# Performance work log

Hardware: AMD Instinct MI355X
Metric: run time of the kernel (lower is better)

The kernel has to match this reference:

```python
import jax, jax.numpy as jnp
import numpy as np
import math

B, N, DQK, DV, M = 8, 8192, 128, 128, 256


def _make_omega(m: int, d: int, seed: int = 0) -> jnp.ndarray:
    """Block-orthogonal random feature matrix, shape [d, m] (matches torch _omega)."""
    rng = np.random.default_rng(seed)
    blocks = []
    nblocks = m // d
    for _ in range(nblocks):
        q, _ = np.linalg.qr(rng.standard_normal((d, d)))
        blocks.append(q.T)
    missing = m - nblocks * d
    if missing > 0:
        q, _ = np.linalg.qr(rng.standard_normal((d, d)))
        blocks.append(q.T[:missing])
    norm = np.linalg.norm(rng.standard_normal((m, d)), axis=1, keepdims=True)
    omega = (norm * np.vstack(blocks)).T  # [d, m]
    return jnp.asarray(omega, dtype=jnp.float32)


def setup_inputs() -> dict:
    key = jax.random.key(0)
    kq, kk, kv = jax.random.split(key, 3)
    Q = jax.random.normal(kq, (B, N, DQK), jnp.float32)
    K = jax.random.normal(kk, (B, N, DQK), jnp.float32)
    V = jax.random.normal(kv, (B, N, DV), jnp.float32)
    atom_mask = jnp.ones((B, N), jnp.float32)
    omega = _make_omega(M, DQK)
    return {"Q": Q, "K": K, "V": V, "atom_mask": atom_mask, "omega": omega}


def _phi(X, mask, omega, is_query: bool, eps: float = 1e-4):
    """Project into random-feature space with Performer stabilization."""
    d = X.shape[-1]
    m = omega.shape[-1]
    U = (X / d ** 0.25) @ omega                       # [B, N, m]
    h = jnp.sum(X * X, axis=-1, keepdims=True) / (2.0 * d ** 0.5)
    if is_query:
        mx = jnp.max(U, axis=-1, keepdims=True)       # per-token max
    else:
        mx = jnp.max(U, axis=(-2, -1), keepdims=True)  # per-batch max
    return (jnp.exp(U - h - mx) + eps) / math.sqrt(m) * mask[..., None]


def reference(Q, K, V, atom_mask, omega):
    eps = 1e-8
    Qp = _phi(Q, atom_mask, omega, True)   # [B, N, M]
    Kp = _phi(K, atom_mask, omega, False)  # [B, N, M]
    # norm_n = Qp_n . sum_j Kp_j
    norm = jnp.einsum('bnm,bm->bn', Qp, jnp.sum(Kp, axis=1))[..., None] + eps
    KV = jnp.einsum('bnm,bnv->bmv', Kp, V)             # [B, M, DV]
    return jnp.einsum('bnm,bmv->bnv', Qp, KV) / norm   # [B, N, DV]
```

## Files before the change

### kernel.cpp

```cpp
#include <hip/hip_runtime.h>
#include <math.h>

#define BB 8
#define NN 8192
#define DD 128
#define MM 256
#define DVV 128
#define PP 32
#define CHUNK 32

#define XSCALE 0.29730177875068026f
#define INV_SQRT_M 0.0625f

typedef _Float16 f16x8 __attribute__((ext_vector_type(8)));
typedef float f32x16 __attribute__((ext_vector_type(16)));

#define FR(s, l) ((s) * 520 + (l) * 8)

__device__ __forceinline__ unsigned f2ord(float f) {
    unsigned u = __float_as_uint(f);
    return (u & 0x80000000u) ? ~u : (u | 0x80000000u);
}
__device__ __forceinline__ float ord2f(unsigned u) {
    return (u & 0x80000000u) ? __uint_as_float(u & 0x7fffffffu) : __uint_as_float(~u);
}
__device__ __forceinline__ f32x16 mfma16(f16x8 a, f16x8 b, f32x16 c) {
    return __builtin_amdgcn_mfma_f32_32x32x16_f16(a, b, c, 0, 0, 0);
}
__device__ __forceinline__ int rowf(int r, int q) { return (r & 3) + 8 * (r >> 2) + 4 * q; }

__device__ __forceinline__ void stage_A(const float* __restrict__ src,
                                        _Float16* R1, float* hs, float* msk,
                                        const float* __restrict__ mrow, bool do_h) {
    const int tid = threadIdx.x;
    const int t = tid >> 3, ks = tid & 7;
    const float4* s4 = (const float4*)(src + t * DD + ks * 16);
    float x[16];
    #pragma unroll
    for (int u = 0; u < 4; ++u) {
        float4 v = s4[u];
        x[u*4+0] = v.x * XSCALE; x[u*4+1] = v.y * XSCALE;
        x[u*4+2] = v.z * XSCALE; x[u*4+3] = v.w * XSCALE;
    }
    if (do_h) {
        float p = 0.f;
        #pragma unroll
        for (int u = 0; u < 16; ++u) p += x[u] * x[u];
        p += __shfl_xor(p, 1, 64); p += __shfl_xor(p, 2, 64); p += __shfl_xor(p, 4, 64);
        if (ks == 0) { hs[t] = 0.5f * p; msk[t] = mrow[t]; }
    }
    #pragma unroll
    for (int q = 0; q < 2; ++q) {
        f16x8 h8, l8;
        #pragma unroll
        for (int j = 0; j < 8; ++j) {
            float xv = x[q*8 + j];
            _Float16 h = (_Float16)xv;
            h8[j] = h; l8[j] = (_Float16)(xv - (float)h);
        }
        *(f16x8*)&R1[FR(0*8 + ks, q*32 + t)] = h8;
        *(f16x8*)&R1[FR(1*8 + ks, q*32 + t)] = l8;
    }
}

__device__ __forceinline__ void stage_BV(const float* __restrict__ src, _Float16* R1) {
    const int tid = threadIdx.x;
    const int t = tid >> 3, c0 = (tid & 7) * 16;
    const int ts = t >> 4, qq = (t >> 3) & 1, j = t & 7;
    const float4* s4 = (const float4*)(src + t * DVV + c0);
    #pragma unroll
    for (int u = 0; u < 4; ++u) {
        float4 v = s4[u];
        float vv[4] = {v.x, v.y, v.z, v.w};
        #pragma unroll
        for (int e = 0; e < 4; ++e) {
            int c = c0 + u*4 + e;
            int vt = c >> 5, iv = c & 31;
            _Float16 h = (_Float16)vv[e];
            R1[FR((0*4 + vt)*2 + ts, qq*32 + iv) + j] = h;
            R1[FR((1*4 + vt)*2 + ts, qq*32 + iv) + j] = (_Float16)(vv[e] - (float)h);
        }
    }
}

__global__ __launch_bounds__(256) void pack_kernel(const float* __restrict__ omega,
                                                   _Float16* __restrict__ omh,
                                                   _Float16* __restrict__ oml,
                                                   unsigned* __restrict__ kmaxord) {
    int g = blockIdx.x * 256 + threadIdx.x;
    if (g < BB) kmaxord[g] = f2ord(-INFINITY);
    int lane = g & 63, ks = (g >> 6) & 7, nt = g >> 9;
    int q = lane >> 5, i = lane & 31;
    f16x8 h8, l8;
    #pragma unroll
    for (int j = 0; j < 8; ++j) {
        float w = omega[(size_t)(ks*16 + q*8 + j) * MM + nt*32 + i];
        _Float16 h = (_Float16)w;
        h8[j] = h; l8[j] = (_Float16)(w - (float)h);
    }
    ((f16x8*)omh)[g] = h8;
    ((f16x8*)oml)[g] = l8;
}

__global__ __launch_bounds__(256, 2) void kmax_kernel(const float* __restrict__ K,
                                                      const _Float16* __restrict__ omh,
                                                      unsigned* __restrict__ kmaxord) {
    __shared__ __align__(16) _Float16 R1[16 * 520];
    __shared__ float wred[4];
    const int b = blockIdx.y;
    const int tid = threadIdx.x, w = tid >> 6, lane = tid & 63;

    f16x8 om[2][8];
    #pragma unroll
    for (int n = 0; n < 2; ++n)
        #pragma unroll
        for (int k = 0; k < 8; ++k)
            om[n][k] = ((const f16x8*)omh)[((2*w + n)*8 + k)*64 + lane];

    float mx = -INFINITY;
    for (int c = 0; c < 8; ++c) {
        int t0 = (blockIdx.x * 8 + c) * CHUNK;
        __syncthreads();
        stage_A(K + ((size_t)b*NN + t0) * DD, R1, nullptr, nullptr, nullptr, false);
        __syncthreads();
        f32x16 a0, a1;
        #pragma unroll
        for (int r = 0; r < 16; ++r) { a0[r] = 0.f; a1[r] = 0.f; }
        #pragma unroll
        for (int ks = 0; ks < 8; ++ks) {
            f16x8 ah = *(const f16x8*)&R1[FR(ks, lane)];
            a0 = mfma16(ah, om[0][ks], a0);
            a1 = mfma16(ah, om[1][ks], a1);
        }
        #pragma unroll
        for (int r = 0; r < 16; ++r) mx = fmaxf(mx, fmaxf(a0[r], a1[r]));
    }
    #pragma unroll
    for (int off = 1; off < 64; off <<= 1) mx = fmaxf(mx, __shfl_xor(mx, off, 64));
    if (lane == 0) wred[w] = mx;
    __syncthreads();
    if (tid == 0)
        atomicMax(kmaxord + b,
                  f2ord(fmaxf(fmaxf(wred[0], wred[1]), fmaxf(wred[2], wred[3]))));
}

__global__ __launch_bounds__(256) void kv_kernel(const float* __restrict__ K,
                                                 const float* __restrict__ V,
                                                 const float* __restrict__ mask,
                                                 const _Float16* __restrict__ omh,
                                                 const _Float16* __restrict__ oml,
                                                 const unsigned* __restrict__ kmaxord,
                                                 float* __restrict__ pkv,
                                                 float* __restrict__ pks) {
    __shared__ __align__(16) _Float16 R1[16 * 520];
    __shared__ __align__(16) _Float16 R2[32 * 520];
    __shared__ float hs[32], msk[32];
    const int b = blockIdx.y, p = blockIdx.x;
    const int tid = threadIdx.x, w = tid >> 6, lane = tid & 63;
    const int i = tid & 31, q = (tid >> 5) & 1;
    const float kmaxv = ord2f(kmaxord[b]);

    f16x8 omf[2][2][8];
    #pragma unroll
    for (int n = 0; n < 2; ++n)
        #pragma unroll
        for (int k = 0; k < 8; ++k) {
            omf[0][n][k] = ((const f16x8*)omh)[((2*w + n)*8 + k)*64 + lane];
            omf[1][n][k] = ((const f16x8*)oml)[((2*w + n)*8 + k)*64 + lane];
        }

    f32x16 kvacc[2][4];
    #pragma unroll
    for (int f = 0; f < 2; ++f)
        #pragma unroll
        for (int vt = 0; vt < 4; ++vt)
            #pragma unroll
            for (int r = 0; r < 16; ++r) kvacc[f][vt][r] = 0.f;
    float ksa[2] = {0.f, 0.f};

    for (int c = 0; c < 8; ++c) {
        int t0 = (p * 8 + c) * CHUNK;
        __syncthreads();
        stage_A(K + ((size_t)b*NN + t0) * DD, R1, hs, msk,
                mask + (size_t)b*NN + t0, true);
        __syncthreads();

        f32x16 a0, a1;
        #pragma unroll
        for (int r = 0; r < 16; ++r) { a0[r] = 0.f; a1[r] = 0.f; }
        #pragma unroll
        for (int ks = 0; ks < 8; ++ks) {
            f16x8 ah = *(const f16x8*)&R1[FR(ks, lane)];
            f16x8 al = *(const f16x8*)&R1[FR(8 + ks, lane)];
            a0 = mfma16(ah, omf[0][0][ks], a0);
            a0 = mfma16(ah, omf[1][0][ks], a0);
            a0 = mfma16(al, omf[0][0][ks], a0);
            a1 = mfma16(ah, omf[0][1][ks], a1);
            a1 = mfma16(ah, omf[1][1][ks], a1);
            a1 = mfma16(al, omf[0][1][ks], a1);
        }
        __syncthreads();

        stage_BV(V + ((size_t)b*NN + t0) * DVV, R1);
        #pragma unroll
        for (int r = 0; r < 16; ++r) {
            int tok = rowf(r, q);
            float hh = hs[tok] + kmaxv;
            float mm = msk[tok] * INV_SQRT_M;
            int ts = tok >> 4, qq = (tok >> 3) & 1, j = tok & 7;
            {
                float kp = (__expf(a0[r] - hh) + 1e-4f) * mm;
                ksa[0] += kp;
                _Float16 h = (_Float16)kp;
                R2[FR((2*w + 0)*2 + ts, qq*32 + i) + j] = h;
                R2[FR(16 + (2*w + 0)*2 + ts, qq*32 + i) + j] = (_Float16)(kp - (float)h);
            }
            {
                float kp = (__expf(a1[r] - hh) + 1e-4f) * mm;
                ksa[1] += kp;
                _Float16 h = (_Float16)kp;
                R2[FR((2*w + 1)*2 + ts, qq*32 + i) + j] = h;
                R2[FR(16 + (2*w + 1)*2 + ts, qq*32 + i) + j] = (_Float16)(kp - (float)h);
            }
        }
        __syncthreads();

        #pragma unroll
        for (int f = 0; f < 2; ++f) {
            int ft = 2*w + f;
            f16x8 ah[2], al[2];
            #pragma unroll
            for (int ts = 0; ts < 2; ++ts) {
                ah[ts] = *(const f16x8*)&R2[FR(ft*2 + ts, lane)];
                al[ts] = *(const f16x8*)&R2[FR(16 + ft*2 + ts, lane)];
            }
            #pragma unroll
            for (int vt = 0; vt < 4; ++vt) {
                #pragma unroll
                for (int ts = 0; ts < 2; ++ts) {
                    f16x8 bh = *(const f16x8*)&R1[FR(vt*2 + ts, lane)];
                    f16x8 bl = *(const f16x8*)&R1[FR(8 + vt*2 + ts, lane)];
                    kvacc[f][vt] = mfma16(ah[ts], bh, kvacc[f][vt]);
                    kvacc[f][vt] = mfma16(ah[ts], bl, kvacc[f][vt]);
                    kvacc[f][vt] = mfma16(al[ts], bh, kvacc[f][vt]);
                }
            }
        }
    }

    float* dst = pkv + ((size_t)(b * PP + p) << 15);
    #pragma unroll
    for (int f = 0; f < 2; ++f)
        #pragma unroll
        for (int vt = 0; vt < 4; ++vt)
            #pragma unroll
            for (int r = 0; r < 16; ++r) {
                int feat = (2*w + f)*32 + rowf(r, q);
                dst[feat * DVV + vt*32 + i] = kvacc[f][vt][r];
            }
    #pragma unroll
    for (int n = 0; n < 2; ++n) {
        float s = ksa[n] + __shfl_xor(ksa[n], 32, 64);
        if (q == 0) pks[(size_t)(b * PP + p) * MM + (2*w + n)*32 + i] = s;
    }
}

__global__ __launch_bounds__(256) void reduce_kernel(const float* __restrict__ pkv,
                                                     const float* __restrict__ pks,
                                                     float* __restrict__ ksum,
                                                     _Float16* __restrict__ kvph,
                                                     _Float16* __restrict__ kvpl) {
    const int b = blockIdx.y;
    int g = blockIdx.x * 256 + threadIdx.x;
    float s = 0.f;
    for (int p = 0; p < PP; ++p) s += pkv[((size_t)(b * PP + p) << 15) + g];
    int f = g >> 7, v = g & 127;
    int vt = v >> 5, iv = v & 31, fs = f >> 4, qq = (f >> 3) & 1, j = f & 7;
    size_t idx = (size_t)b * 32768 + (size_t)((vt*16 + fs)*64 + qq*32 + iv)*8 + j;
    _Float16 h = (_Float16)s;
    kvph[idx] = h;
    kvpl[idx] = (_Float16)(s - (float)h);
    if (blockIdx.x == 0) {
        float ss = 0.f;
        for (int p = 0; p < PP; ++p) ss += pks[(size_t)(b * PP + p) * MM + g];
        ksum[b * MM + g] = ss;
    }
}

__global__ __launch_bounds__(256) void out_kernel(const float* __restrict__ Q,
                                                  const float* __restrict__ mask,
                                                  const _Float16* __restrict__ omh,
                                                  const _Float16* __restrict__ oml,
                                                  const float* __restrict__ ksum,
                                                  const _Float16* __restrict__ kvph,
                                                  const _Float16* __restrict__ kvpl,
                                                  float* __restrict__ out) {
    __shared__ __align__(16) _Float16 R1[16 * 520];
    __shared__ __align__(16) _Float16 R2[32 * 520];
    __shared__ float hs[32], msk[32], wmax[4][32], norms[32];
    const int b = blockIdx.y;
    const int tid = threadIdx.x, w = tid >> 6, lane = tid & 63;
    const int i = tid & 31, q = (tid >> 5) & 1;

    f16x8 omf[2][2][8];
    #pragma unroll
    for (int n = 0; n < 2; ++n)
        #pragma unroll
        for (int k = 0; k < 8; ++k) {
            omf[0][n][k] = ((const f16x8*)omh)[((2*w + n)*8 + k)*64 + lane];
            omf[1][n][k] = ((const f16x8*)oml)[((2*w + n)*8 + k)*64 + lane];
        }
    f16x8 bfh[16], bfl[16];
    #pragma unroll
    for (int fs = 0; fs < 16; ++fs) {
        bfh[fs] = ((const f16x8*)kvph)[(size_t)b * 4096 + (w*16 + fs)*64 + lane];
        bfl[fs] = ((const f16x8*)kvpl)[(size_t)b * 4096 + (w*16 + fs)*64 + lane];
    }
    f16x8 bnh[4], bnl[4];
    #pragma unroll
    for (int u = 0; u < 4; ++u) {
        f16x8 hh, ll;
        #pragma unroll
        for (int j = 0; j < 8; ++j) { hh[j] = (_Float16)0.f; ll[j] = (_Float16)0.f; }
        if (i == 0) {
            #pragma unroll
            for (int j = 0; j < 8; ++j) {
                float s = ksum[b * MM + (4*w + u)*16 + q*8 + j];
                _Float16 h = (_Float16)s;
                hh[j] = h; ll[j] = (_Float16)(s - (float)h);
            }
        }
        bnh[u] = hh; bnl[u] = ll;
    }

    for (int c = 0; c < 8; ++c) {
        int t0 = (blockIdx.x * 8 + c) * CHUNK;
        __syncthreads();
        stage_A(Q + ((size_t)b*NN + t0) * DD, R1, hs, msk,
                mask + (size_t)b*NN + t0, true);
        if (tid < 32) norms[tid] = 1e-8f;
        __syncthreads();

        f32x16 a0, a1;
        #pragma unroll
        for (int r = 0; r < 16; ++r) { a0[r] = 0.f; a1[r] = 0.f; }
        #pragma unroll
        for (int ks = 0; ks < 8; ++ks) {
            f16x8 ah = *(const f16x8*)&R1[FR(ks, lane)];
            f16x8 al = *(const f16x8*)&R1[FR(8 + ks, lane)];
            a0 = mfma16(ah, omf[0][0][ks], a0);
            a0 = mfma16(ah, omf[1][0][ks], a0);
            a0 = mfma16(al, omf[0][0][ks], a0);
            a1 = mfma16(ah, omf[0][1][ks], a1);
            a1 = mfma16(ah, omf[1][1][ks], a1);
            a1 = mfma16(al, omf[0][1][ks], a1);
        }
        float tm[16];
        #pragma unroll
        for (int r = 0; r < 16; ++r) tm[r] = fmaxf(a0[r], a1[r]);
        #pragma unroll
        for (int off = 1; off < 32; off <<= 1)
            #pragma unroll
            for (int r = 0; r < 16; ++r) tm[r] = fmaxf(tm[r], __shfl_xor(tm[r], off, 64));
        if (i == 0)
            #pragma unroll
            for (int r = 0; r < 16; ++r) wmax[w][rowf(r, q)] = tm[r];
        __syncthreads();

        #pragma unroll
        for (int r = 0; r < 16; ++r) {
            int tok = rowf(r, q);
            float tmax = fmaxf(fmaxf(wmax[0][tok], wmax[1][tok]),
                               fmaxf(wmax[2][tok], wmax[3][tok]));
            float hh = hs[tok] + tmax;
            float mm = msk[tok] * INV_SQRT_M;
            #pragma unroll
            for (int n = 0; n < 2; ++n) {
                float qp = (__expf((n ? a1[r] : a0[r]) - hh) + 1e-4f) * mm;
                int feat = (2*w + n)*32 + i;
                int fstep = feat >> 4, fq = (i >> 3) & 1, fj = i & 7;
                _Float16 h = (_Float16)qp;
                R2[FR(fstep, fq*32 + tok) + fj] = h;
                R2[FR(16 + fstep, fq*32 + tok) + fj] = (_Float16)(qp - (float)h);
            }
        }
        __syncthreads();

        f32x16 oa, na;
        #pragma unroll
        for (int r = 0; r < 16; ++r) { oa[r] = 0.f; na[r] = 0.f; }
        #pragma unroll
        for (int fs = 0; fs < 16; ++fs) {
            f16x8 ah = *(const f16x8*)&R2[FR(fs, lane)];
            f16x8 al = *(const f16x8*)&R2[FR(16 + fs, lane)];
            oa = mfma16(ah, bfh[fs], oa);
            oa = mfma16(ah, bfl[fs], oa);
            oa = mfma16(al, bfh[fs], oa);
        }
        #pragma unroll
        for (int u = 0; u < 4; ++u) {
            f16x8 ah = *(const f16x8*)&R2[FR(4*w + u, lane)];
            f16x8 al = *(const f16x8*)&R2[FR(16 + 4*w + u, lane)];
            na = mfma16(ah, bnh[u], na);
            na = mfma16(ah, bnl[u], na);
            na = mfma16(al, bnh[u], na);
        }
        if (i == 0)
            #pragma unroll
            for (int r = 0; r < 16; ++r) atomicAdd(&norms[rowf(r, q)], na[r]);
        __syncthreads();

        float* ob = out + ((size_t)b*NN + t0) * DVV + w*32 + i;
        #pragma unroll
        for (int r = 0; r < 16; ++r) {
            int tok = rowf(r, q);
            ob[(size_t)tok * DVV] = oa[r] / norms[tok];
        }
    }
}

extern "C" void kernel_launch(void* const* d_in, const int* in_sizes, int n_in,
                              void* d_out, int out_size, void* d_ws, size_t ws_size,
                              hipStream_t stream) {
    const float* Q     = (const float*)d_in[0];
    const float* K     = (const float*)d_in[1];
    const float* V     = (const float*)d_in[2];
    const float* mask  = (const float*)d_in[3];
    const float* omega = (const float*)d_in[4];
    float* out = (float*)d_out;

    char* ws = (char*)d_ws;
    _Float16* omh    = (_Float16*)(ws);
    _Float16* oml    = (_Float16*)(ws + (64 << 10));
    unsigned* kmaxord = (unsigned*)(ws + (128 << 10));
    float*    ksum   = (float*)(ws + (132 << 10));
    float*    pks    = (float*)(ws + (140 << 10));
    _Float16* kvph   = (_Float16*)(ws + (400 << 10));
    _Float16* kvpl   = (_Float16*)(ws + (912 << 10));
    float*    pkv    = (float*)(ws + (2 << 20));

    pack_kernel<<<16, 256, 0, stream>>>(omega, omh, oml, kmaxord);
    kmax_kernel<<<dim3(32, BB), 256, 0, stream>>>(K, omh, kmaxord);
    kv_kernel<<<dim3(PP, BB), 256, 0, stream>>>(K, V, mask, omh, oml, kmaxord, pkv, pks);
    reduce_kernel<<<dim3(128, BB), 256, 0, stream>>>(pkv, pks, ksum, kvph, kvpl);
    out_kernel<<<dim3(32, BB), 256, 0, stream>>>(Q, mask, omh, oml, ksum, kvph, kvpl, out);
}
```

Measured before the change: 250.5 us.

## Split feature tiles across blocks and drop register-resident omega/KV fragments

kmax and kv kernels now split the 256 random features across two blocks via a new grid dimension, so each wave handles one 32-feature tile instead of two. That halves accumulators and shared R2 and allows higher occupancy through launch bounds. out_kernel gets four times more blocks (two chunks each) and streams omega and KV fragments from global/L2 inside the loop instead of keeping them in registers. The cost is redundant K/V staging per feature half and more global loads per chunk, in exchange for more resident waves and better latency hiding.

```diff
diff --git a/kernel.cpp b/kernel.cpp
--- a/kernel.cpp
+++ b/kernel.cpp
@@ -102,20 +102,19 @@
     ((f16x8*)oml)[g] = l8;
 }
 
-__global__ __launch_bounds__(256, 2) void kmax_kernel(const float* __restrict__ K,
+__global__ __launch_bounds__(256, 4) void kmax_kernel(const float* __restrict__ K,
                                                       const _Float16* __restrict__ omh,
                                                       unsigned* __restrict__ kmaxord) {
     __shared__ __align__(16) _Float16 R1[16 * 520];
     __shared__ float wred[4];
-    const int b = blockIdx.y;
+    const int b = blockIdx.z;
     const int tid = threadIdx.x, w = tid >> 6, lane = tid & 63;
-
-    f16x8 om[2][8];
-    #pragma unroll
-    for (int n = 0; n < 2; ++n)
-        #pragma unroll
-        for (int k = 0; k < 8; ++k)
-            om[n][k] = ((const f16x8*)omh)[((2*w + n)*8 + k)*64 + lane];
+    const int nt = blockIdx.y * 4 + w;
+
+    f16x8 om[8];
+    #pragma unroll
+    for (int k = 0; k < 8; ++k)
+        om[k] = ((const f16x8*)omh)[(nt*8 + k)*64 + lane];
 
     float mx = -INFINITY;
     for (int c = 0; c < 8; ++c) {
@@ -123,17 +122,16 @@
         __syncthreads();
         stage_A(K + ((size_t)b*NN + t0) * DD, R1, nullptr, nullptr, nullptr, false);
         __syncthreads();
-        f32x16 a0, a1;
-        #pragma unroll
-        for (int r = 0; r < 16; ++r) { a0[r] = 0.f; a1[r] = 0.f; }
+        f32x16 a0;
+        #pragma unroll
+        for (int r = 0; r < 16; ++r) a0[r] = 0.f;
         #pragma unroll
         for (int ks = 0; ks < 8; ++ks) {
             f16x8 ah = *(const f16x8*)&R1[FR(ks, lane)];
-            a0 = mfma16(ah, om[0][ks], a0);
-            a1 = mfma16(ah, om[1][ks], a1);
-        }
-        #pragma unroll
-        for (int r = 0; r < 16; ++r) mx = fmaxf(mx, fmaxf(a0[r], a1[r]));
+            a0 = mfma16(ah, om[ks], a0);
+        }
+        #pragma unroll
+        for (int r = 0; r < 16; ++r) mx = fmaxf(mx, a0[r]);
     }
     #pragma unroll
     for (int off = 1; off < 64; off <<= 1) mx = fmaxf(mx, __shfl_xor(mx, off, 64));
@@ -144,39 +142,31 @@
                   f2ord(fmaxf(fmaxf(wred[0], wred[1]), fmaxf(wred[2], wred[3]))));
 }
 
-__global__ __launch_bounds__(256) void kv_kernel(const float* __restrict__ K,
-                                                 const float* __restrict__ V,
-                                                 const float* __restrict__ mask,
-                                                 const _Float16* __restrict__ omh,
-                                                 const _Float16* __restrict__ oml,
-                                                 const unsigned* __restrict__ kmaxord,
-                                                 float* __restrict__ pkv,
-                                                 float* __restrict__ pks) {
+__global__ __launch_bounds__(256, 3) void kv_kernel(const float* __restrict__ K,
+                                                    const float* __restrict__ V,
+                                                    const float* __restrict__ mask,
+                                                    const _Float16* __restrict__ omh,
+                                                    const _Float16* __restrict__ oml,
+                                                    const unsigned* __restrict__ kmaxord,
+                                                    float* __restrict__ pkv,
+                                                    float* __restrict__ pks) {
     __shared__ __align__(16) _Float16 R1[16 * 520];
-    __shared__ __align__(16) _Float16 R2[32 * 520];
+    __shared__ __align__(16) _Float16 R2[16 * 520];
     __shared__ float hs[32], msk[32];
-    const int b = blockIdx.y, p = blockIdx.x;
+    const int b = blockIdx.z, p = blockIdx.x;
     const int tid = threadIdx.x, w = tid >> 6, lane = tid & 63;
     const int i = tid & 31, q = (tid >> 5) & 1;
+    const int nt = blockIdx.y * 4 + w;
     const float kmaxv = ord2f(kmaxord[b]);
-
-    f16x8 omf[2][2][8];
-    #pragma unroll
-    for (int n = 0; n < 2; ++n)
-        #pragma unroll
-        for (int k = 0; k < 8; ++k) {
-            omf[0][n][k] = ((const f16x8*)omh)[((2*w + n)*8 + k)*64 + lane];
-            omf[1][n][k] = ((const f16x8*)oml)[((2*w + n)*8 + k)*64 + lane];
-        }
-
-    f32x16 kvacc[2][4];
-    #pragma unroll
-    for (int f = 0; f < 2; ++f)
-        #pragma unroll
-        for (int vt = 0; vt < 4; ++vt)
-            #pragma unroll
-            for (int r = 0; r < 16; ++r) kvacc[f][vt][r] = 0.f;
-    float ksa[2] = {0.f, 0.f};
+    const f16x8* om4h = (const f16x8*)omh;
+    const f16x8* om4l = (const f16x8*)oml;
+
+    f32x16 kvacc[4];
+    #pragma unroll
+    for (int vt = 0; vt < 4; ++vt)
+        #pragma unroll
+        for (int r = 0; r < 16; ++r) kvacc[vt][r] = 0.f;
+    float ksa = 0.f;
 
     for (int c = 0; c < 8; ++c) {
         int t0 = (p * 8 + c) * CHUNK;
@@ -185,19 +175,18 @@
                 mask + (size_t)b*NN + t0, true);
         __syncthreads();
 
-        f32x16 a0, a1;
-        #pragma unroll
-        for (int r = 0; r < 16; ++r) { a0[r] = 0.f; a1[r] = 0.f; }
+        f32x16 a0;
+        #pragma unroll
+        for (int r = 0; r < 16; ++r) a0[r] = 0.f;
         #pragma unroll
         for (int ks = 0; ks < 8; ++ks) {
+            f16x8 oh = om4h[(nt*8 + ks)*64 + lane];
+            f16x8 ol = om4l[(nt*8 + ks)*64 + lane];
             f16x8 ah = *(const f16x8*)&R1[FR(ks, lane)];
             f16x8 al = *(const f16x8*)&R1[FR(8 + ks, lane)];
-            a0 = mfma16(ah, omf[0][0][ks], a0);
-            a0 = mfma16(ah, omf[1][0][ks], a0);
-            a0 = mfma16(al, omf[0][0][ks], a0);
-            a1 = mfma16(ah, omf[0][1][ks], a1);
-            a1 = mfma16(ah, omf[1][1][ks], a1);
-            a1 = mfma16(al, omf[0][1][ks], a1);
+            a0 = mfma16(ah, oh, a0);
+            a0 = mfma16(ah, ol, a0);
+            a0 = mfma16(al, oh, a0);
         }
         __syncthreads();
 
@@ -208,60 +197,44 @@
             float hh = hs[tok] + kmaxv;
             float mm = msk[tok] * INV_SQRT_M;
             int ts = tok >> 4, qq = (tok >> 3) & 1, j = tok & 7;
-            {
-                float kp = (__expf(a0[r] - hh) + 1e-4f) * mm;
-                ksa[0] += kp;
-                _Float16 h = (_Float16)kp;
-                R2[FR((2*w + 0)*2 + ts, qq*32 + i) + j] = h;
-                R2[FR(16 + (2*w + 0)*2 + ts, qq*32 + i) + j] = (_Float16)(kp - (float)h);
+            float kp = (__expf(a0[r] - hh) + 1e-4f) * mm;
+            ksa += kp;
+            _Float16 h = (_Float16)kp;
+            R2[FR(w*4 + ts, qq*32 + i) + j] = h;
+            R2[FR(w*4 + 2 + ts, qq*32 + i) + j] = (_Float16)(kp - (float)h);
+        }
+        __syncthreads();
+
+        f16x8 ah[2], al[2];
+        #pragma unroll
+        for (int ts = 0; ts < 2; ++ts) {
+            ah[ts] = *(const f16x8*)&R2[FR(w*4 + ts, lane)];
+            al[ts] = *(const f16x8*)&R2[FR(w*4 + 2 + ts, lane)];
+        }
+        #pragma unroll
+        for (int vt = 0; vt < 4; ++vt) {
+            #pragma unroll
+            for (int ts = 0; ts < 2; ++ts) {
+                f16x8 bh = *(const f16x8*)&R1[FR(vt*2 + ts, lane)];
+                f16x8 bl = *(const f16x8*)&R1[FR(8 + vt*2 + ts, lane)];
+                kvacc[vt] = mfma16(ah[ts], bh, kvacc[vt]);
+                kvacc[vt] = mfma16(ah[ts], bl, kvacc[vt]);
+                kvacc[vt] = mfma16(al[ts], bh, kvacc[vt]);
             }
-            {
-                float kp = (__expf(a1[r] - hh) + 1e-4f) * mm;
-                ksa[1] += kp;
-                _Float16 h = (_Float16)kp;
-                R2[FR((2*w + 1)*2 + ts, qq*32 + i) + j] = h;
-                R2[FR(16 + (2*w + 1)*2 + ts, qq*32 + i) + j] = (_Float16)(kp - (float)h);
-            }
-        }
-        __syncthreads();
-
-        #pragma unroll
-        for (int f = 0; f < 2; ++f) {
-            int ft = 2*w + f;
-            f16x8 ah[2], al[2];
-            #pragma unroll
-            for (int ts = 0; ts < 2; ++ts) {
-                ah[ts] = *(const f16x8*)&R2[FR(ft*2 + ts, lane)];
-                al[ts] = *(const f16x8*)&R2[FR(16 + ft*2 + ts, lane)];
-            }
-            #pragma unroll
-            for (int vt = 0; vt < 4; ++vt) {
-                #pragma unroll
-                for (int ts = 0; ts < 2; ++ts) {
-                    f16x8 bh = *(const f16x8*)&R1[FR(vt*2 + ts, lane)];
-                    f16x8 bl = *(const f16x8*)&R1[FR(8 + vt*2 + ts, lane)];
-                    kvacc[f][vt] = mfma16(ah[ts], bh, kvacc[f][vt]);
-                    kvacc[f][vt] = mfma16(ah[ts], bl, kvacc[f][vt]);
-                    kvacc[f][vt] = mfma16(al[ts], bh, kvacc[f][vt]);
-                }
-            }
         }
     }
 
     float* dst = pkv + ((size_t)(b * PP + p) << 15);
     #pragma unroll
-    for (int f = 0; f < 2; ++f)
-        #pragma unroll
-        for (int vt = 0; vt < 4; ++vt)
-            #pragma unroll
-            for (int r = 0; r < 16; ++r) {
-                int feat = (2*w + f)*32 + rowf(r, q);
-                dst[feat * DVV + vt*32 + i] = kvacc[f][vt][r];
-            }
-    #pragma unroll
-    for (int n = 0; n < 2; ++n) {
-        float s = ksa[n] + __shfl_xor(ksa[n], 32, 64);
-        if (q == 0) pks[(size_t)(b * PP + p) * MM + (2*w + n)*32 + i] = s;
+    for (int vt = 0; vt < 4; ++vt)
+        #pragma unroll
+        for (int r = 0; r < 16; ++r) {
+            int feat = nt*32 + rowf(r, q);
+            dst[feat * DVV + vt*32 + i] = kvacc[vt][r];
+        }
+    {
+        float s = ksa + __shfl_xor(ksa, 32, 64);
+        if (q == 0) pks[(size_t)(b * PP + p) * MM + nt*32 + i] = s;
     }
 }
 
@@ -287,35 +260,25 @@
     }
 }
 
-__global__ __launch_bounds__(256) void out_kernel(const float* __restrict__ Q,
-                                                  const float* __restrict__ mask,
-                                                  const _Float16* __restrict__ omh,
-                                                  const _Float16* __restrict__ oml,
-                                                  const float* __restrict__ ksum,
-                                                  const _Float16* __restrict__ kvph,
-                                                  const _Float16* __restrict__ kvpl,
-                                                  float* __restrict__ out) {
+__global__ __launch_bounds__(256, 3) void out_kernel(const float* __restrict__ Q,
+                                                     const float* __restrict__ mask,
+                                                     const _Float16* __restrict__ omh,
+                                                     const _Float16* __restrict__ oml,
+                                                     const float* __restrict__ ksum,
+                                                     const _Float16* __restrict__ kvph,
+                                                     const _Float16* __restrict__ kvpl,
+                                                     float* __restrict__ out) {
     __shared__ __align__(16) _Float16 R1[16 * 520];
     __shared__ __align__(16) _Float16 R2[32 * 520];
     __shared__ float hs[32], msk[32], wmax[4][32], norms[32];
     const int b = blockIdx.y;
     const int tid = threadIdx.x, w = tid >> 6, lane = tid & 63;
     const int i = tid & 31, q = (tid >> 5) & 1;
-
-    f16x8 omf[2][2][8];
-    #pragma unroll
-    for (int n = 0; n < 2; ++n)
-        #pragma unroll
-        for (int k = 0; k < 8; ++k) {
-            omf[0][n][k] = ((const f16x8*)omh)[((2*w + n)*8 + k)*64 + lane];
-            omf[1][n][k] = ((const f16x8*)oml)[((2*w + n)*8 + k)*64 + lane];
-        }
-    f16x8 bfh[16], bfl[16];
-    #pragma unroll
-    for (int fs = 0; fs < 16; ++fs) {
-        bfh[fs] = ((const f16x8*)kvph)[(size_t)b * 4096 + (w*16 + fs)*64 + lane];
-        bfl[fs] = ((const f16x8*)kvpl)[(size_t)b * 4096 + (w*16 + fs)*64 + lane];
-    }
+    const f16x8* om4h = (const f16x8*)omh;
+    const f16x8* om4l = (const f16x8*)oml;
+    const f16x8* kvh4 = (const f16x8*)kvph;
+    const f16x8* kvl4 = (const f16x8*)kvpl;
+
     f16x8 bnh[4], bnl[4];
     #pragma unroll
     for (int u = 0; u < 4; ++u) {
@@ -333,8 +296,8 @@
         bnh[u] = hh; bnl[u] = ll;
     }
 
-    for (int c = 0; c < 8; ++c) {
-        int t0 = (blockIdx.x * 8 + c) * CHUNK;
+    for (int c = 0; c < 2; ++c) {
+        int t0 = (blockIdx.x * 2 + c) * CHUNK;
         __syncthreads();
         stage_A(Q + ((size_t)b*NN + t0) * DD, R1, hs, msk,
                 mask + (size_t)b*NN + t0, true);
@@ -346,14 +309,18 @@
         for (int r = 0; r < 16; ++r) { a0[r] = 0.f; a1[r] = 0.f; }
         #pragma unroll
         for (int ks = 0; ks < 8; ++ks) {
+            f16x8 o0h = om4h[((2*w + 0)*8 + ks)*64 + lane];
+            f16x8 o0l = om4l[((2*w + 0)*8 + ks)*64 + lane];
+            f16x8 o1h = om4h[((2*w + 1)*8 + ks)*64 + lane];
+            f16x8 o1l = om4l[((2*w + 1)*8 + ks)*64 + lane];
             f16x8 ah = *(const f16x8*)&R1[FR(ks, lane)];
             f16x8 al = *(const f16x8*)&R1[FR(8 + ks, lane)];
-            a0 = mfma16(ah, omf[0][0][ks], a0);
-            a0 = mfma16(ah, omf[1][0][ks], a0);
-            a0 = mfma16(al, omf[0][0][ks], a0);
-            a1 = mfma16(ah, omf[0][1][ks], a1);
-            a1 = mfma16(ah, omf[1][1][ks], a1);
-            a1 = mfma16(al, omf[0][1][ks], a1);
+            a0 = mfma16(ah, o0h, a0);
+            a0 = mfma16(ah, o0l, a0);
+            a0 = mfma16(al, o0h, a0);
+            a1 = mfma16(ah, o1h, a1);
+            a1 = mfma16(ah, o1l, a1);
+            a1 = mfma16(al, o1h, a1);
         }
         float tm[16];
         #pragma unroll
@@ -391,11 +358,13 @@
         for (int r = 0; r < 16; ++r) { oa[r] = 0.f; na[r] = 0.f; }
         #pragma unroll
         for (int fs = 0; fs < 16; ++fs) {
+            f16x8 bh = kvh4[(size_t)b * 4096 + (w*16 + fs)*64 + lane];
+            f16x8 bl = kvl4[(size_t)b * 4096 + (w*16 + fs)*64 + lane];
             f16x8 ah = *(const f16x8*)&R2[FR(fs, lane)];
             f16x8 al = *(const f16x8*)&R2[FR(16 + fs, lane)];
-            oa = mfma16(ah, bfh[fs], oa);
-            oa = mfma16(ah, bfl[fs], oa);
-            oa = mfma16(al, bfh[fs], oa);
+            oa = mfma16(ah, bh, oa);
+            oa = mfma16(ah, bl, oa);
+            oa = mfma16(al, bh, oa);
         }
         #pragma unroll
         for (int u = 0; u < 4; ++u) {
@@ -440,8 +409,8 @@
     float*    pkv    = (float*)(ws + (2 << 20));
 
     pack_kernel<<<16, 256, 0, stream>>>(omega, omh, oml, kmaxord);
-    kmax_kernel<<<dim3(32, BB), 256, 0, stream>>>(K, omh, kmaxord);
-    kv_kernel<<<dim3(PP, BB), 256, 0, stream>>>(K, V, mask, omh, oml, kmaxord, pkv, pks);
+    kmax_kernel<<<dim3(32, 2, BB), 256, 0, stream>>>(K, omh, kmaxord);
+    kv_kernel<<<dim3(PP, 2, BB), 256, 0, stream>>>(K, V, mask, omh, oml, kmaxord, pkv, pks);
     reduce_kernel<<<dim3(128, BB), 256, 0, stream>>>(pkv, pks, ksum, kvph, kvpl);
-    out_kernel<<<dim3(32, BB), 256, 0, stream>>>(Q, mask, omh, oml, ksum, kvph, kvpl, out);
-}
+    out_kernel<<<dim3(128, BB), 256, 0, stream>>>(Q, mask, omh, oml, ksum, kvph, kvpl, out);
+}
```

New measurement: 496.7 us. +98.3%, slower.
